# Kernel tuning notes

Measured on AMD Instinct MI355X. Metric: run time of the kernel, lower is better.

## Reference

```python
import jax, jax.numpy as jnp
import numpy as np

N = 100000   # nodes
E = 1000000  # edges
F = 16       # node features
FE = 4       # edge features
H = 8        # heads
C = 8        # hidden per head
HC = H * C   # 64
G = 64       # graphs in batch
NC = 4       # num classes
NS = 0.2     # negative slope
EPS = 1e-5


def setup_inputs() -> dict:
    key = jax.random.key(0)
    ks = list(jax.random.split(key, 40))
    it = iter(ks)
    nk = lambda shape, scale=0.1: jax.random.normal(next(it), shape, jnp.float32) * scale
    inp = {}
    inp["x"] = jax.random.normal(next(it), (N, F), jnp.float32)
    inp["edge_index"] = jax.random.randint(next(it), (2, E), 0, N, dtype=jnp.int64)
    inp["edge_attr"] = jax.random.normal(next(it), (E, FE), jnp.float32)
    inp["batch"] = jnp.sort(jax.random.randint(next(it), (N,), 0, G, dtype=jnp.int64))
    inp["g_n"] = jnp.ones((F,), jnp.float32); inp["b_n"] = jnp.zeros((F,), jnp.float32)
    inp["g_e"] = jnp.ones((FE,), jnp.float32); inp["b_e"] = jnp.zeros((FE,), jnp.float32)
    dims = [F, HC, HC]
    for i, d in enumerate(dims):
        inp[f"Wl{i}"] = nk((d, HC)); inp[f"bl{i}"] = jnp.zeros((HC,), jnp.float32)
        inp[f"Wr{i}"] = nk((d, HC)); inp[f"br{i}"] = jnp.zeros((HC,), jnp.float32)
        inp[f"We{i}"] = nk((FE, HC))
        inp[f"att{i}"] = nk((H, C))
        inp[f"bc{i}"] = jnp.zeros((HC,), jnp.float32)
    inp["t"] = jnp.ones((), jnp.float32)
    inp["W_out"] = nk((HC, NC)); inp["b_out"] = jnp.zeros((NC,), jnp.float32)
    return inp


def _bn(v, g, b):
    # torch BatchNorm1d training-mode forward: biased batch stats
    m = v.mean(0)
    var = jnp.var(v, 0)
    return (v - m) / jnp.sqrt(var + EPS) * g + b


def reference(x, edge_index, edge_attr, batch, g_n, b_n, g_e, b_e,
              Wl0, bl0, Wr0, br0, We0, att0, bc0,
              Wl1, bl1, Wr1, br1, We1, att1, bc1,
              Wl2, bl2, Wr2, br2, We2, att2, bc2,
              t, W_out, b_out):
    x = _bn(x, g_n, b_n)
    ea = _bn(edge_attr, g_e, b_e)
    src0, dst0 = edge_index[0], edge_index[1]
    # GATv2Conv default add_self_loops=True, fill_value='mean':
    # self-loop edge_attr = mean of incoming edge attrs per node (0 if none)
    cnt = jax.ops.segment_sum(jnp.ones((E,), jnp.float32), dst0, N)
    loop_attr = jax.ops.segment_sum(ea, dst0, N) / jnp.maximum(cnt, 1.0)[:, None]
    ar = jnp.arange(N, dtype=edge_index.dtype)
    src = jnp.concatenate([src0, ar])
    dst = jnp.concatenate([dst0, ar])
    ea_aug = jnp.concatenate([ea, loop_attr], 0)  # [E+N, FE]

    def conv(h, Wl, bl, Wr, br, We, att, bc):
        xl = (h @ Wl + bl).reshape(N, H, C)  # source transform
        xr = (h @ Wr + br).reshape(N, H, C)  # target transform
        ee = (ea_aug @ We).reshape(-1, H, C)
        m = jax.nn.leaky_relu(xl[src] + xr[dst] + ee, NS)  # [E+N, H, C]
        logits = jnp.einsum('ehc,hc->eh', m, att)
        amax = jax.ops.segment_max(logits, dst, N)  # every node has a self loop
        w = jnp.exp(logits - amax[dst])
        den = jax.ops.segment_sum(w, dst, N)
        alpha = w / den[dst]  # edge softmax per target node per head
        out = jax.ops.segment_sum(alpha[:, :, None] * xl[src], dst, N)
        return out.reshape(N, HC) + bc

    layers = [(Wl0, bl0, Wr0, br0, We0, att0, bc0),
              (Wl1, bl1, Wr1, br1, We1, att1, bc1),
              (Wl2, bl2, Wr2, br2, We2, att2, bc2)]
    for p in layers:
        x = jax.nn.leaky_relu(conv(x, *p), NS)

    # learnable softmax readout per graph, elementwise over channels
    s = x * t
    amax = jax.ops.segment_max(s, batch, G)
    w = jnp.exp(s - amax[batch])
    den = jax.ops.segment_sum(w, batch, G)
    agg = jax.ops.segment_sum((w / den[batch]) * x, batch, G)  # [G, HC]
    return agg @ W_out + b_out
```

## Files before the change

kernel.cpp:

```cpp
#include <hip/hip_runtime.h>
#include <math.h>

#define TPB 256
#define NBX 256
#define NBE 1024
#define CONVB 2048

typedef unsigned short u16;

__device__ __forceinline__ float lrelu(float v){ return fmaxf(v, 0.2f*v); }
#define RF(x) __builtin_amdgcn_readfirstlane(x)

__device__ __forceinline__ unsigned pack_bf16(float a, float b){
  unsigned ua = __float_as_uint(a), ub = __float_as_uint(b);
  ua = (ua + 0x7FFFu + ((ua >> 16) & 1u)) >> 16;
  ub = (ub + 0x7FFFu + ((ub >> 16) & 1u)) >> 16;
  return ua | (ub << 16);
}

__global__ __launch_bounds__(TPB) void k_stats_x(const float* __restrict__ x, float* __restrict__ px, int n){
  __shared__ float lds[4*32];
  int tid = blockIdx.x*blockDim.x + threadIdx.x;
  int stride = gridDim.x*blockDim.x;
  float s[16], q[16];
  #pragma unroll
  for (int i=0;i<16;++i){ s[i]=0.f; q[i]=0.f; }
  for (int r=tid; r<n; r+=stride){
    const float4* p = (const float4*)(x + (long)r*16);
    #pragma unroll
    for (int j=0;j<4;++j){
      float4 v = p[j];
      s[j*4+0]+=v.x; q[j*4+0]+=v.x*v.x;
      s[j*4+1]+=v.y; q[j*4+1]+=v.y*v.y;
      s[j*4+2]+=v.z; q[j*4+2]+=v.z*v.z;
      s[j*4+3]+=v.w; q[j*4+3]+=v.w*v.w;
    }
  }
  int wid = threadIdx.x >> 6, lane = threadIdx.x & 63;
  #pragma unroll
  for (int i=0;i<32;++i){
    float v = (i<16) ? s[i] : q[i-16];
    #pragma unroll
    for (int m=1;m<64;m<<=1) v += __shfl_xor(v, m);
    if (lane==0) lds[wid*32+i] = v;
  }
  __syncthreads();
  if (threadIdx.x < 32){
    float v = lds[threadIdx.x] + lds[32+threadIdx.x] + lds[64+threadIdx.x] + lds[96+threadIdx.x];
    px[blockIdx.x*32 + threadIdx.x] = v;
  }
}

__global__ __launch_bounds__(TPB) void k_edge0(const float* __restrict__ ea, const int* __restrict__ ei,
                      float* __restrict__ pe, int* __restrict__ cnt, int* __restrict__ rank, int E){
  __shared__ float lds[4*8];
  int tid = blockIdx.x*blockDim.x + threadIdx.x;
  int stride = gridDim.x*blockDim.x;
  float s[4]={0,0,0,0}, q[4]={0,0,0,0};
  for (int r=tid; r<E; r+=stride){
    float4 v = ((const float4*)ea)[r];
    s[0]+=v.x; q[0]+=v.x*v.x;
    s[1]+=v.y; q[1]+=v.y*v.y;
    s[2]+=v.z; q[2]+=v.z*v.z;
    s[3]+=v.w; q[3]+=v.w*v.w;
    int d = ei[E + r];
    rank[r] = atomicAdd(&cnt[d], 1);
  }
  int wid = threadIdx.x >> 6, lane = threadIdx.x & 63;
  #pragma unroll
  for (int i=0;i<8;++i){
    float v = (i<4) ? s[i] : q[i-4];
    #pragma unroll
    for (int m=1;m<64;m<<=1) v += __shfl_xor(v, m);
    if (lane==0) lds[wid*8+i] = v;
  }
  __syncthreads();
  if (threadIdx.x < 8){
    float v = lds[threadIdx.x] + lds[8+threadIdx.x] + lds[16+threadIdx.x] + lds[24+threadIdx.x];
    pe[blockIdx.x*8 + threadIdx.x] = v;
  }
}

__global__ __launch_bounds__(TPB) void k_finalize(const float* __restrict__ g_n, const float* __restrict__ b_n,
                           const float* __restrict__ g_e, const float* __restrict__ b_e,
                           const float* __restrict__ px, const float* __restrict__ pe,
                           float* __restrict__ st, int n, int e){
  __shared__ float lx[256], le[256];
  int t = threadIdx.x;
  {
    int c = t & 31, ch = t >> 5;
    float sx = 0.f;
    for (int b = ch*32; b < ch*32+32; ++b) sx += px[b*32 + c];
    lx[t] = sx;
  }
  {
    int c = t & 7, ch = t >> 3;
    float se = 0.f;
    for (int b = ch*32; b < ch*32+32; ++b) se += pe[b*8 + c];
    le[t] = se;
  }
  __syncthreads();
  if (t < 16){
    float sum = 0.f, sq = 0.f;
    #pragma unroll
    for (int ch=0; ch<8; ++ch){ sum += lx[ch*32 + t]; sq += lx[ch*32 + 16 + t]; }
    float mean = sum / (float)n;
    float var  = sq / (float)n - mean*mean;
    float sc = g_n[t] * rsqrtf(var + 1e-5f);
    st[40+t] = sc; st[56+t] = b_n[t] - mean*sc;
  } else if (t < 20){
    int f = t-16;
    float sum = 0.f, sq = 0.f;
    #pragma unroll
    for (int ch=0; ch<32; ++ch){ sum += le[ch*8 + f]; sq += le[ch*8 + 4 + f]; }
    float mean = sum / (float)e;
    float var  = sq / (float)e - mean*mean;
    float sc = g_e[f] * rsqrtf(var + 1e-5f);
    st[72+f] = sc; st[76+f] = b_e[f] - mean*sc;
  }
}

__global__ __launch_bounds__(TPB) void k_scan_a(const int* __restrict__ cnt, int* __restrict__ rp,
                                                int* __restrict__ part, int n){
  __shared__ int lds[TPB];
  int t = threadIdx.x;
  int base = blockIdx.x*2048 + t*8;
  int v[8]; int run = 0;
  #pragma unroll
  for (int j=0;j<8;++j){
    int idx = base + j;
    v[j] = run;
    run += (idx < n) ? cnt[idx] : 0;
  }
  lds[t] = run;
  __syncthreads();
  for (int off=1; off<TPB; off<<=1){
    int add = (t >= off) ? lds[t-off] : 0;
    __syncthreads();
    lds[t] += add;
    __syncthreads();
  }
  int excl = lds[t] - run;
  if (t == TPB-1) part[blockIdx.x] = lds[t];
  #pragma unroll
  for (int j=0;j<8;++j){
    int idx = base + j;
    if (idx < n) rp[idx] = v[j] + excl + idx;
  }
}

__global__ void k_scan_b(int* __restrict__ part, int nb){
  if (threadIdx.x==0 && blockIdx.x==0){
    int run = 0;
    for (int i=0;i<nb;++i){ int v = part[i]; part[i] = run; run += v; }
    part[nb] = run;
  }
}

__global__ __launch_bounds__(TPB) void k_scan_c(int* __restrict__ rp, const int* __restrict__ part, int n, int nb){
  int idx = blockIdx.x*blockDim.x + threadIdx.x;
  if (idx < n) rp[idx] += part[idx >> 11];
  else if (idx == n) rp[n] = part[nb] + n;
}

__global__ __launch_bounds__(TPB) void k_scatter(const int* __restrict__ ei, const int* __restrict__ rank,
                        const int* __restrict__ rp, int2* __restrict__ csr_se, int E){
  for (int e = blockIdx.x*blockDim.x + threadIdx.x; e < E; e += gridDim.x*blockDim.x){
    int srcv = ei[e];
    int d    = ei[E + e];
    int pos = rp[d] + rank[e];
    csr_se[pos] = make_int2(srcv, e);
  }
}

__global__ __launch_bounds__(TPB) void k_post(const int2* __restrict__ csr_se, const float4* __restrict__ ea,
                        const float* __restrict__ st, const int* __restrict__ rp,
                        int* __restrict__ csr_src, float4* __restrict__ csr_ea, int n){
  int lane = threadIdx.x & 63;
  int l16 = lane & 15;
  int node = (blockIdx.x*4 + (threadIdx.x >> 6))*4 + (lane >> 4);
  if (node >= n) return;
  float s0=st[72], s1=st[73], s2=st[74], s3=st[75];
  float h0=st[76], h1=st[77], h2=st[78], h3=st[79];
  int ib = rp[node], ie1 = rp[node+1] - 1;
  float4 sum = make_float4(0.f,0.f,0.f,0.f);
  for (int i = ib + l16; i < ie1; i += 16){
    int2 se = csr_se[i];
    float4 v = ea[se.y];
    float4 nv = make_float4(fmaf(v.x,s0,h0), fmaf(v.y,s1,h1), fmaf(v.z,s2,h2), fmaf(v.w,s3,h3));
    csr_src[i] = se.x;
    csr_ea[i] = nv;
    sum.x += nv.x; sum.y += nv.y; sum.z += nv.z; sum.w += nv.w;
  }
  #pragma unroll
  for (int m=1;m<16;m<<=1){
    sum.x += __shfl_xor(sum.x, m);
    sum.y += __shfl_xor(sum.y, m);
    sum.z += __shfl_xor(sum.z, m);
    sum.w += __shfl_xor(sum.w, m);
  }
  if (l16 == 0){
    int deg = ie1 - ib;
    float ic = 1.f / fmaxf((float)deg, 1.f);
    csr_src[ie1] = node;
    csr_ea[ie1] = make_float4(sum.x*ic, sum.y*ic, sum.z*ic, sum.w*ic);
  }
}

#define FMA16(i, xv) {                          \
    acc[i][0]  = fmaf(xv, wa.x, acc[i][0]);     \
    acc[i][1]  = fmaf(xv, wa.y, acc[i][1]);     \
    acc[i][2]  = fmaf(xv, wa.z, acc[i][2]);     \
    acc[i][3]  = fmaf(xv, wa.w, acc[i][3]);     \
    acc[i][4]  = fmaf(xv, wb.x, acc[i][4]);     \
    acc[i][5]  = fmaf(xv, wb.y, acc[i][5]);     \
    acc[i][6]  = fmaf(xv, wb.z, acc[i][6]);     \
    acc[i][7]  = fmaf(xv, wb.w, acc[i][7]);     \
    acc[i][8]  = fmaf(xv, wc.x, acc[i][8]);     \
    acc[i][9]  = fmaf(xv, wc.y, acc[i][9]);     \
    acc[i][10] = fmaf(xv, wc.z, acc[i][10]);    \
    acc[i][11] = fmaf(xv, wc.w, acc[i][11]);    \
    acc[i][12] = fmaf(xv, wd.x, acc[i][12]);    \
    acc[i][13] = fmaf(xv, wd.y, acc[i][13]);    \
    acc[i][14] = fmaf(xv, wd.z, acc[i][14]);    \
    acc[i][15] = fmaf(xv, wd.w, acc[i][15]); }
#define KSTEP(kk, c0_, c1_, c2_, c3_) {                                        \
    const float4* w4 = (const float4*)&Wlds[(k4*4+kk)*128 + c16];              \
    float4 wa = w4[0], wb = w4[1], wc = w4[2], wd = w4[3];                     \
    FMA16(0, c0_); FMA16(1, c1_); FMA16(2, c2_); FMA16(3, c3_); }

template<int K, bool BN>
__global__ __launch_bounds__(TPB) void k_gemm(const float* __restrict__ X,
    const float* __restrict__ Wl, const float* __restrict__ bl,
    const float* __restrict__ Wr, const float* __restrict__ br,
    const float* __restrict__ st,
    u16* __restrict__ xl, float* __restrict__ xr, int nrows){
  __shared__ __align__(16) float Wlds[K*128];
  __shared__ float blds[128];
  __shared__ float bns[16], bnb[16];
  int t = threadIdx.x;
  for (int idx = t; idx < K*128; idx += TPB){
    int k = idx >> 7, j = idx & 127;
    Wlds[idx] = (j < 64) ? Wl[k*64 + j] : Wr[k*64 + (j - 64)];
  }
  if (t < 64) blds[t] = bl[t];
  else if (t < 128) blds[t] = br[t - 64];
  if (BN){ if (t >= 128 && t < 144){ bns[t-128] = st[40 + (t-128)]; bnb[t-128] = st[56 + (t-128)]; } }
  __syncthreads();
  int rg = t & 31, c = t >> 5;
  int c16 = c*16;
  int r0 = blockIdx.x*128 + rg*4;
  int r[4];
  #pragma unroll
  for (int i=0;i<4;++i){ int ri = r0 + i; r[i] = (ri < nrows) ? ri : (nrows-1); }
  float acc[4][16];
  #pragma unroll
  for (int i=0;i<4;++i){
    #pragma unroll
    for (int j=0;j<16;++j) acc[i][j]=0.f;
  }
  #pragma unroll 2
  for (int k4=0; k4<K/4; ++k4){
    float4 xa = *(const float4*)&X[(size_t)r[0]*K + k4*4];
    float4 xb = *(const float4*)&X[(size_t)r[1]*K + k4*4];
    float4 xc = *(const float4*)&X[(size_t)r[2]*K + k4*4];
    float4 xd = *(const float4*)&X[(size_t)r[3]*K + k4*4];
    if (BN){
      float s0=bns[k4*4+0], b0=bnb[k4*4+0];
      float s1=bns[k4*4+1], b1=bnb[k4*4+1];
      float s2=bns[k4*4+2], b2=bnb[k4*4+2];
      float s3=bns[k4*4+3], b3=bnb[k4*4+3];
      xa.x=fmaf(xa.x,s0,b0); xa.y=fmaf(xa.y,s1,b1); xa.z=fmaf(xa.z,s2,b2); xa.w=fmaf(xa.w,s3,b3);
      xb.x=fmaf(xb.x,s0,b0); xb.y=fmaf(xb.y,s1,b1); xb.z=fmaf(xb.z,s2,b2); xb.w=fmaf(xb.w,s3,b3);
      xc.x=fmaf(xc.x,s0,b0); xc.y=fmaf(xc.y,s1,b1); xc.z=fmaf(xc.z,s2,b2); xc.w=fmaf(xc.w,s3,b3);
      xd.x=fmaf(xd.x,s0,b0); xd.y=fmaf(xd.y,s1,b1); xd.z=fmaf(xd.z,s2,b2); xd.w=fmaf(xd.w,s3,b3);
    }
    KSTEP(0, xa.x, xb.x, xc.x, xd.x);
    KSTEP(1, xa.y, xb.y, xc.y, xd.y);
    KSTEP(2, xa.z, xb.z, xc.z, xd.z);
    KSTEP(3, xa.w, xb.w, xc.w, xd.w);
  }
  if (c16 < 64){
    #pragma unroll
    for (int i=0;i<4;++i){
      if (r0 + i < nrows){
        u16* qb = &xl[(size_t)(r0+i)*64 + c16];
        uint4 p0, p1;
        p0.x = pack_bf16(acc[i][0] +blds[c16+0],  acc[i][1] +blds[c16+1]);
        p0.y = pack_bf16(acc[i][2] +blds[c16+2],  acc[i][3] +blds[c16+3]);
        p0.z = pack_bf16(acc[i][4] +blds[c16+4],  acc[i][5] +blds[c16+5]);
        p0.w = pack_bf16(acc[i][6] +blds[c16+6],  acc[i][7] +blds[c16+7]);
        p1.x = pack_bf16(acc[i][8] +blds[c16+8],  acc[i][9] +blds[c16+9]);
        p1.y = pack_bf16(acc[i][10]+blds[c16+10], acc[i][11]+blds[c16+11]);
        p1.z = pack_bf16(acc[i][12]+blds[c16+12], acc[i][13]+blds[c16+13]);
        p1.w = pack_bf16(acc[i][14]+blds[c16+14], acc[i][15]+blds[c16+15]);
        ((uint4*)qb)[0] = p0;
        ((uint4*)qb)[1] = p1;
      }
    }
  } else {
    int cb = c16 - 64;
    #pragma unroll
    for (int i=0;i<4;++i){
      if (r0 + i < nrows){
        float* q = &xr[(size_t)(r0+i)*64 + cb];
        ((float4*)q)[0] = make_float4(acc[i][0]+blds[c16+0],  acc[i][1]+blds[c16+1],
                                      acc[i][2]+blds[c16+2],  acc[i][3]+blds[c16+3]);
        ((float4*)q)[1] = make_float4(acc[i][4]+blds[c16+4],  acc[i][5]+blds[c16+5],
                                      acc[i][6]+blds[c16+6],  acc[i][7]+blds[c16+7]);
        ((float4*)q)[2] = make_float4(acc[i][8]+blds[c16+8],  acc[i][9]+blds[c16+9],
                                      acc[i][10]+blds[c16+10],acc[i][11]+blds[c16+11]);
        ((float4*)q)[3] = make_float4(acc[i][12]+blds[c16+12],acc[i][13]+blds[c16+13],
                                      acc[i][14]+blds[c16+14],acc[i][15]+blds[c16+15]);
      }
    }
  }
}

#define PROC(e_, a_, S_, O_) {                                              \
    float v = a_ + xrv;                                                     \
    v = fmaf(e_.x,we0, fmaf(e_.y,we1, fmaf(e_.z,we2, fmaf(e_.w,we3, v))));  \
    v = lrelu(v);                                                           \
    float p = v*attv;                                                       \
    p += __shfl_xor(p,1); p += __shfl_xor(p,2); p += __shfl_xor(p,4);       \
    float w_ = __expf(p);                                                   \
    S_ += w_; O_ = fmaf(w_, a_, O_); }
#define LOADSLOT(e_, a_, idx) { int s_ = RF(csr_src[idx]); e_ = csr_ea[idx]; \
    a_ = __uint_as_float(((unsigned)xl[(size_t)s_*64 + lane]) << 16); }

__global__ __launch_bounds__(TPB) void k_conv(
    const u16* __restrict__ xl, const float* __restrict__ xr,
    const int* __restrict__ rp, const int* __restrict__ csr_src, const float4* __restrict__ csr_ea,
    const float* __restrict__ We, const float* __restrict__ att, const float* __restrict__ bc,
    float* __restrict__ xout, int n){
  int lane = threadIdx.x & 63;
  int gw = blockIdx.x*4 + (threadIdx.x >> 6);
  int nw = gridDim.x*4;
  float we0 = We[lane], we1 = We[64+lane], we2 = We[128+lane], we3 = We[192+lane];
  float attv = att[lane];
  float bcv  = bc[lane];

  for (int node = gw; node < n; node += nw){
    int ib = RF(rp[node]);
    int ie = RF(rp[node+1]);
    float xrv = xr[(size_t)node*64 + lane];
    int ln = ie - ib;
    float S0=0.f, O0=0.f, S1=0.f, O1=0.f;
    float4 e0, e1, e2, e3, e4, e5;
    float a0=0.f, a1=0.f, a2=0.f, a3=0.f, a4=0.f, a5=0.f;
    LOADSLOT(e0, a0, ib);
    if (ln > 1) LOADSLOT(e1, a1, ib+1);
    if (ln > 2) LOADSLOT(e2, a2, ib+2);
    if (ln > 3) LOADSLOT(e3, a3, ib+3);
    if (ln > 4) LOADSLOT(e4, a4, ib+4);
    if (ln > 5) LOADSLOT(e5, a5, ib+5);
    int i = ib;
    for (; i+6 <= ie; i += 6){
      PROC(e0, a0, S0, O0); if (i+6  < ie) LOADSLOT(e0, a0, i+6);
      PROC(e1, a1, S1, O1); if (i+7  < ie) LOADSLOT(e1, a1, i+7);
      PROC(e2, a2, S0, O0); if (i+8  < ie) LOADSLOT(e2, a2, i+8);
      PROC(e3, a3, S1, O1); if (i+9  < ie) LOADSLOT(e3, a3, i+9);
      PROC(e4, a4, S0, O0); if (i+10 < ie) LOADSLOT(e4, a4, i+10);
      PROC(e5, a5, S1, O1); if (i+11 < ie) LOADSLOT(e5, a5, i+11);
    }
    int r = ie - i;
    if (r > 0) PROC(e0, a0, S0, O0);
    if (r > 1) PROC(e1, a1, S1, O1);
    if (r > 2) PROC(e2, a2, S0, O0);
    if (r > 3) PROC(e3, a3, S1, O1);
    if (r > 4) PROC(e4, a4, S0, O0);
    float o = (O0 + O1) / (S0 + S1) + bcv;
    xout[(size_t)node*64 + lane] = lrelu(o);
  }
}

__global__ __launch_bounds__(1024) void k_readout(const float* __restrict__ x,
    const int* __restrict__ batch, const float* __restrict__ tin,
    const float* __restrict__ Wout, const float* __restrict__ bout,
    float* __restrict__ out, int n){
  int g = blockIdx.x;
  int lane = threadIdx.x & 63, wid = threadIdx.x >> 6;
  int lo, hi;
  { int a=0, b=n; while (a<b){ int m=(a+b)>>1; if (batch[m] <  g) a=m+1; else b=m; } lo=a; }
  { int a=lo, b=n; while (a<b){ int m=(a+b)>>1; if (batch[m] <= g) a=m+1; else b=m; } hi=a; }
  float t = tin[0];
  __shared__ float red[16][64];
  float mx = -INFINITY;
  for (int nd = lo + wid; nd < hi; nd += 16)
    mx = fmaxf(mx, x[(size_t)nd*64 + lane]*t);
  red[wid][lane] = mx;
  __syncthreads();
  mx = -INFINITY;
  #pragma unroll
  for (int wv=0; wv<16; ++wv) mx = fmaxf(mx, red[wv][lane]);
  __syncthreads();
  float ld = 0.f, ln = 0.f;
  for (int nd = lo + wid; nd < hi; nd += 16){
    float xv = x[(size_t)nd*64 + lane];
    float w = __expf(xv*t - mx);
    ld += w; ln = fmaf(w, xv, ln);
  }
  red[wid][lane] = ld;
  __syncthreads();
  float den = 0.f;
  #pragma unroll
  for (int wv=0; wv<16; ++wv) den += red[wv][lane];
  __syncthreads();
  red[wid][lane] = ln;
  __syncthreads();
  if (wid == 0){
    float num = 0.f;
    #pragma unroll
    for (int wv=0; wv<16; ++wv) num += red[wv][lane];
    float agg = (hi > lo) ? num/den : 0.f;
    #pragma unroll
    for (int c=0;c<4;++c){
      float p = agg * Wout[lane*4 + c];
      #pragma unroll
      for (int m=1;m<64;m<<=1) p += __shfl_xor(p, m);
      if (lane == 0) out[g*4 + c] = p + bout[c];
    }
  }
}

extern "C" void kernel_launch(void* const* d_in, const int* in_sizes, int n_in,
                              void* d_out, int out_size, void* d_ws, size_t ws_size,
                              hipStream_t stream){
  const float* x     = (const float*)d_in[0];
  const int*   ei    = (const int*)d_in[1];
  const float* ea    = (const float*)d_in[2];
  const int*   batch = (const int*)d_in[3];
  const float* g_n = (const float*)d_in[4];
  const float* b_n = (const float*)d_in[5];
  const float* g_e = (const float*)d_in[6];
  const float* b_e = (const float*)d_in[7];
  const float* Wl[3]  = {(const float*)d_in[8],  (const float*)d_in[15], (const float*)d_in[22]};
  const float* bl[3]  = {(const float*)d_in[9],  (const float*)d_in[16], (const float*)d_in[23]};
  const float* Wr[3]  = {(const float*)d_in[10], (const float*)d_in[17], (const float*)d_in[24]};
  const float* br[3]  = {(const float*)d_in[11], (const float*)d_in[18], (const float*)d_in[25]};
  const float* We[3]  = {(const float*)d_in[12], (const float*)d_in[19], (const float*)d_in[26]};
  const float* att[3] = {(const float*)d_in[13], (const float*)d_in[20], (const float*)d_in[27]};
  const float* bc[3]  = {(const float*)d_in[14], (const float*)d_in[21], (const float*)d_in[28]};
  const float* tin  = (const float*)d_in[29];
  const float* Wout = (const float*)d_in[30];
  const float* bout = (const float*)d_in[31];
  float* out = (float*)d_out;

  const int n = in_sizes[0] / 16;
  const int E = in_sizes[1] / 2;

  char* w = (char*)d_ws;
  size_t off = 0;
  auto alloc = [&](size_t bytes)->char*{
    char* p = w + off;
    off = (off + bytes + 255) & ~(size_t)255;
    return p;
  };
  int*      cnt      = (int*)alloc((size_t)n*4);
  size_t zero_end = off;
  float*    st       = (float*)alloc(128*4);
  int*      rank     = (int*)alloc((size_t)E*4);
  float*    px       = (float*)alloc((size_t)NBX*32*4);
  float*    pe       = (float*)alloc((size_t)NBE*8*4);
  int*      rp       = (int*)alloc(((size_t)n+1)*4);
  int*      part     = (int*)alloc(64*4);
  int2*     csr_se   = (int2*)alloc((size_t)(E+n)*8);
  int*      csr_src  = (int*)alloc((size_t)(E+n)*4);
  float4*   csr_ea   = (float4*)alloc((size_t)(E+n)*16);
  u16*      xlb      = (u16*)alloc((size_t)n*64*2);
  float*    xrb      = (float*)alloc((size_t)n*64*4);
  float*    xbuf     = (float*)alloc((size_t)n*64*4);
  if (off > ws_size) return;

  hipMemsetAsync(d_ws, 0, zero_end, stream);

  k_stats_x<<<NBX, TPB, 0, stream>>>(x, px, n);
  k_edge0<<<NBE, TPB, 0, stream>>>(ea, ei, pe, cnt, rank, E);
  k_finalize<<<1, TPB, 0, stream>>>(g_n, b_n, g_e, b_e, px, pe, st, n, E);
  int nb = (n + 2047) / 2048;
  k_scan_a<<<nb, TPB, 0, stream>>>(cnt, rp, part, n);
  k_scan_b<<<1, 1, 0, stream>>>(part, nb);
  k_scan_c<<<(n + 1 + TPB - 1)/TPB, TPB, 0, stream>>>(rp, part, n, nb);
  k_scatter<<<2048, TPB, 0, stream>>>(ei, rank, rp, csr_se, E);
  k_post<<<(n + 15)/16, TPB, 0, stream>>>(csr_se, (const float4*)ea, st, rp, csr_src, (float4*)csr_ea, n);

  int gb = (n + 127)/128;
  for (int l=0; l<3; ++l){
    if (l == 0)
      k_gemm<16,true><<<gb, TPB, 0, stream>>>(x, Wl[0], bl[0], Wr[0], br[0], st, xlb, xrb, n);
    else
      k_gemm<64,false><<<gb, TPB, 0, stream>>>(xbuf, Wl[l], bl[l], Wr[l], br[l], st, xlb, xrb, n);
    k_conv<<<CONVB, TPB, 0, stream>>>(xlb, xrb, rp, csr_src, csr_ea,
                                      We[l], att[l], bc[l], xbuf, n);
  }

  k_readout<<<64, 1024, 0, stream>>>(xbuf, batch, tin, Wout, bout, out, n);
}
```

Before: 532.0 us.

## Process two edges per wavefront in conv by splitting lanes into half-waves

The attention-aggregation kernel now assigns each half of a 64-lane wavefront a different edge, with each lane handling two channels (packed bf16 pair loads, float2 xr). Partial sums from the two halves are combined with a cross-half shuffle at the end, and odd edge counts are handled by a masked tail. This doubles edges in flight per wave and halves the loop trip count, aiming to cut the latency-bound gather loop. In exchange each lane does more arithmetic per edge, source indices are no longer wave-uniform, and the final reduction adds shuffles.

```diff
diff --git a/kernel.cpp b/kernel.cpp
--- a/kernel.cpp
+++ b/kernel.cpp
@@ -317,16 +317,20 @@
   }
 }
 
-#define PROC(e_, a_, S_, O_) {                                              \
-    float v = a_ + xrv;                                                     \
-    v = fmaf(e_.x,we0, fmaf(e_.y,we1, fmaf(e_.z,we2, fmaf(e_.w,we3, v))));  \
-    v = lrelu(v);                                                           \
-    float p = v*attv;                                                       \
-    p += __shfl_xor(p,1); p += __shfl_xor(p,2); p += __shfl_xor(p,4);       \
-    float w_ = __expf(p);                                                   \
-    S_ += w_; O_ = fmaf(w_, a_, O_); }
-#define LOADSLOT(e_, a_, idx) { int s_ = RF(csr_src[idx]); e_ = csr_ea[idx]; \
-    a_ = __uint_as_float(((unsigned)xl[(size_t)s_*64 + lane]) << 16); }
+#define LOADP(e_, u_, i_) { int idx_ = (i_) + half; int s_ = csr_src[idx_];     \
+    e_ = csr_ea[idx_];                                                          \
+    u_ = *(const unsigned*)&xl[(size_t)s_*64 + (l32<<1)]; }
+#define PROCP(e_, u_) {                                                         \
+    float ax_ = __uint_as_float((u_) << 16);                                    \
+    float ay_ = __uint_as_float((u_) & 0xffff0000u);                            \
+    float v0_ = ax_ + xrx, v1_ = ay_ + xry;                                     \
+    v0_ = fmaf(e_.x,we0x, fmaf(e_.y,we1x, fmaf(e_.z,we2x, fmaf(e_.w,we3x, v0_))));\
+    v1_ = fmaf(e_.x,we0y, fmaf(e_.y,we1y, fmaf(e_.z,we2y, fmaf(e_.w,we3y, v1_))));\
+    v0_ = lrelu(v0_); v1_ = lrelu(v1_);                                         \
+    float p_ = fmaf(v0_, attx, v1_*atty);                                       \
+    p_ += __shfl_xor(p_,1); p_ += __shfl_xor(p_,2);                             \
+    float w_ = __expf(p_);                                                      \
+    S += w_; Ox = fmaf(w_,ax_,Ox); Oy = fmaf(w_,ay_,Oy); }
 
 __global__ __launch_bounds__(TPB) void k_conv(
     const u16* __restrict__ xl, const float* __restrict__ xr,
@@ -334,43 +338,65 @@
     const float* __restrict__ We, const float* __restrict__ att, const float* __restrict__ bc,
     float* __restrict__ xout, int n){
   int lane = threadIdx.x & 63;
+  int half = lane >> 5;
+  int l32  = lane & 31;
+  int c0 = l32*2, c1 = c0+1;
   int gw = blockIdx.x*4 + (threadIdx.x >> 6);
   int nw = gridDim.x*4;
-  float we0 = We[lane], we1 = We[64+lane], we2 = We[128+lane], we3 = We[192+lane];
-  float attv = att[lane];
-  float bcv  = bc[lane];
+  float we0x = We[c0],      we0y = We[c1];
+  float we1x = We[64+c0],   we1y = We[64+c1];
+  float we2x = We[128+c0],  we2y = We[128+c1];
+  float we3x = We[192+c0],  we3y = We[192+c1];
+  float attx = att[c0], atty = att[c1];
+  float bcx  = bc[c0],  bcy  = bc[c1];
 
   for (int node = gw; node < n; node += nw){
     int ib = RF(rp[node]);
     int ie = RF(rp[node+1]);
-    float xrv = xr[(size_t)node*64 + lane];
-    int ln = ie - ib;
-    float S0=0.f, O0=0.f, S1=0.f, O1=0.f;
-    float4 e0, e1, e2, e3, e4, e5;
-    float a0=0.f, a1=0.f, a2=0.f, a3=0.f, a4=0.f, a5=0.f;
-    LOADSLOT(e0, a0, ib);
-    if (ln > 1) LOADSLOT(e1, a1, ib+1);
-    if (ln > 2) LOADSLOT(e2, a2, ib+2);
-    if (ln > 3) LOADSLOT(e3, a3, ib+3);
-    if (ln > 4) LOADSLOT(e4, a4, ib+4);
-    if (ln > 5) LOADSLOT(e5, a5, ib+5);
+    int cnt = ie - ib;
+    float2 xrv = *(const float2*)&xr[(size_t)node*64 + c0];
+    float xrx = xrv.x, xry = xrv.y;
+    float S = 0.f, Ox = 0.f, Oy = 0.f;
+    float4 e0, e1, e2; unsigned u0=0, u1=0, u2=0;
+    int npf = cnt >> 1;
+    int iendf = ib + npf*2;
+    if (npf > 0) LOADP(e0,u0, ib);
+    if (npf > 1) LOADP(e1,u1, ib+2);
+    if (npf > 2) LOADP(e2,u2, ib+4);
     int i = ib;
-    for (; i+6 <= ie; i += 6){
-      PROC(e0, a0, S0, O0); if (i+6  < ie) LOADSLOT(e0, a0, i+6);
-      PROC(e1, a1, S1, O1); if (i+7  < ie) LOADSLOT(e1, a1, i+7);
-      PROC(e2, a2, S0, O0); if (i+8  < ie) LOADSLOT(e2, a2, i+8);
-      PROC(e3, a3, S1, O1); if (i+9  < ie) LOADSLOT(e3, a3, i+9);
-      PROC(e4, a4, S0, O0); if (i+10 < ie) LOADSLOT(e4, a4, i+10);
-      PROC(e5, a5, S1, O1); if (i+11 < ie) LOADSLOT(e5, a5, i+11);
-    }
-    int r = ie - i;
-    if (r > 0) PROC(e0, a0, S0, O0);
-    if (r > 1) PROC(e1, a1, S1, O1);
-    if (r > 2) PROC(e2, a2, S0, O0);
-    if (r > 3) PROC(e3, a3, S1, O1);
-    if (r > 4) PROC(e4, a4, S0, O0);
-    float o = (O0 + O1) / (S0 + S1) + bcv;
-    xout[(size_t)node*64 + lane] = lrelu(o);
+    for (; i+6 <= iendf; i += 6){
+      PROCP(e0,u0); if (i+6  < iendf) LOADP(e0,u0, i+6);
+      PROCP(e1,u1); if (i+8  < iendf) LOADP(e1,u1, i+8);
+      PROCP(e2,u2); if (i+10 < iendf) LOADP(e2,u2, i+10);
+    }
+    int rem = (iendf - i) >> 1;
+    if (rem > 0) PROCP(e0,u0);
+    if (rem > 1) PROCP(e1,u1);
+    if (cnt & 1){
+      int idx_ = min(iendf + half, ie - 1);
+      int s_ = csr_src[idx_];
+      float4 et = csr_ea[idx_];
+      unsigned ut = *(const unsigned*)&xl[(size_t)s_*64 + (l32<<1)];
+      float ax_ = __uint_as_float(ut << 16);
+      float ay_ = __uint_as_float(ut & 0xffff0000u);
+      float v0_ = ax_ + xrx, v1_ = ay_ + xry;
+      v0_ = fmaf(et.x,we0x, fmaf(et.y,we1x, fmaf(et.z,we2x, fmaf(et.w,we3x, v0_))));
+      v1_ = fmaf(et.x,we0y, fmaf(et.y,we1y, fmaf(et.z,we2y, fmaf(et.w,we3y, v1_))));
+      v0_ = lrelu(v0_); v1_ = lrelu(v1_);
+      float p_ = fmaf(v0_, attx, v1_*atty);
+      p_ += __shfl_xor(p_,1); p_ += __shfl_xor(p_,2);
+      float w_ = (half == 0) ? __expf(p_) : 0.f;
+      S += w_; Ox = fmaf(w_,ax_,Ox); Oy = fmaf(w_,ay_,Oy);
+    }
+    S  += __shfl_xor(S, 32);
+    Ox += __shfl_xor(Ox, 32);
+    Oy += __shfl_xor(Oy, 32);
+    if (half == 0){
+      float2 o;
+      o.x = lrelu(Ox / S + bcx);
+      o.y = lrelu(Oy / S + bcy);
+      *(float2*)&xout[(size_t)node*64 + c0] = o;
+    }
   }
 }
 
```

Measured after the change: 452.5 us. 14.9% less time.

## Process four edges per wavefront in GAT conv and fold scan stage into scan_c

Applied to the files above, without the earlier changes.

The conv kernel now splits each 64-lane wavefront into four 16-lane quarters. Each quarter handles a different edge and each lane covers 4 channels, loaded as a packed bf16 uint2, with the partial sums reduced across quarters by shuffles at the end. This cuts the per-edge shuffle chain and the serial dependency on one edge per wave, aiming for better memory-level parallelism on the gathers, in exchange for extra cross-quarter reductions and a masked remainder path. The single-thread k_scan_b launch is also removed: each thread in k_scan_c sums the block partials itself, which is cheap because there are only about 49 chunks.

```diff
diff --git a/kernel.cpp b/kernel.cpp
--- a/kernel.cpp
+++ b/kernel.cpp
@@ -149,18 +149,18 @@
   }
 }
 
-__global__ void k_scan_b(int* __restrict__ part, int nb){
-  if (threadIdx.x==0 && blockIdx.x==0){
-    int run = 0;
-    for (int i=0;i<nb;++i){ int v = part[i]; part[i] = run; run += v; }
-    part[nb] = run;
-  }
-}
-
 __global__ __launch_bounds__(TPB) void k_scan_c(int* __restrict__ rp, const int* __restrict__ part, int n, int nb){
   int idx = blockIdx.x*blockDim.x + threadIdx.x;
-  if (idx < n) rp[idx] += part[idx >> 11];
-  else if (idx == n) rp[n] = part[nb] + n;
+  if (idx < n){
+    int chunk = idx >> 11;
+    int add = 0;
+    for (int b = 0; b < chunk; ++b) add += part[b];
+    rp[idx] += add;
+  } else if (idx == n){
+    int tot = 0;
+    for (int b = 0; b < nb; ++b) tot += part[b];
+    rp[n] = tot + n;
+  }
 }
 
 __global__ __launch_bounds__(TPB) void k_scatter(const int* __restrict__ ei, const int* __restrict__ rank,
@@ -317,16 +317,27 @@
   }
 }
 
-#define PROC(e_, a_, S_, O_) {                                              \
-    float v = a_ + xrv;                                                     \
-    v = fmaf(e_.x,we0, fmaf(e_.y,we1, fmaf(e_.z,we2, fmaf(e_.w,we3, v))));  \
-    v = lrelu(v);                                                           \
-    float p = v*attv;                                                       \
-    p += __shfl_xor(p,1); p += __shfl_xor(p,2); p += __shfl_xor(p,4);       \
-    float w_ = __expf(p);                                                   \
-    S_ += w_; O_ = fmaf(w_, a_, O_); }
-#define LOADSLOT(e_, a_, idx) { int s_ = RF(csr_src[idx]); e_ = csr_ea[idx]; \
-    a_ = __uint_as_float(((unsigned)xl[(size_t)s_*64 + lane]) << 16); }
+#define LOADQ(e_, u_, i_) { int idx_ = (i_) + qq; int s_ = csr_src[idx_];       \
+    e_ = csr_ea[idx_];                                                          \
+    u_ = *(const uint2*)&xl[(size_t)s_*64 + (l16<<2)]; }
+#define PROCQ(e_, u_) {                                                         \
+    float a0_ = __uint_as_float((u_).x << 16);                                  \
+    float a1_ = __uint_as_float((u_).x & 0xffff0000u);                          \
+    float a2_ = __uint_as_float((u_).y << 16);                                  \
+    float a3_ = __uint_as_float((u_).y & 0xffff0000u);                          \
+    float v0_ = a0_ + xr4.x, v1_ = a1_ + xr4.y;                                 \
+    float v2_ = a2_ + xr4.z, v3_ = a3_ + xr4.w;                                 \
+    v0_ = fmaf(e_.x,we0.x, fmaf(e_.y,we1.x, fmaf(e_.z,we2.x, fmaf(e_.w,we3.x, v0_)))); \
+    v1_ = fmaf(e_.x,we0.y, fmaf(e_.y,we1.y, fmaf(e_.z,we2.y, fmaf(e_.w,we3.y, v1_)))); \
+    v2_ = fmaf(e_.x,we0.z, fmaf(e_.y,we1.z, fmaf(e_.z,we2.z, fmaf(e_.w,we3.z, v2_)))); \
+    v3_ = fmaf(e_.x,we0.w, fmaf(e_.y,we1.w, fmaf(e_.z,we2.w, fmaf(e_.w,we3.w, v3_)))); \
+    v0_=lrelu(v0_); v1_=lrelu(v1_); v2_=lrelu(v2_); v3_=lrelu(v3_);             \
+    float p_ = fmaf(v0_,att4.x, fmaf(v1_,att4.y, fmaf(v2_,att4.z, v3_*att4.w))); \
+    p_ += __shfl_xor(p_, 1);                                                    \
+    float w_ = __expf(p_);                                                      \
+    S += w_;                                                                    \
+    O0 = fmaf(w_,a0_,O0); O1 = fmaf(w_,a1_,O1);                                 \
+    O2 = fmaf(w_,a2_,O2); O3 = fmaf(w_,a3_,O3); }
 
 __global__ __launch_bounds__(TPB) void k_conv(
     const u16* __restrict__ xl, const float* __restrict__ xr,
@@ -334,43 +345,73 @@
     const float* __restrict__ We, const float* __restrict__ att, const float* __restrict__ bc,
     float* __restrict__ xout, int n){
   int lane = threadIdx.x & 63;
+  int qq  = lane >> 4;
+  int l16 = lane & 15;
+  int c0 = l16*4;
   int gw = blockIdx.x*4 + (threadIdx.x >> 6);
   int nw = gridDim.x*4;
-  float we0 = We[lane], we1 = We[64+lane], we2 = We[128+lane], we3 = We[192+lane];
-  float attv = att[lane];
-  float bcv  = bc[lane];
+  float4 we0 = *(const float4*)&We[c0];
+  float4 we1 = *(const float4*)&We[64+c0];
+  float4 we2 = *(const float4*)&We[128+c0];
+  float4 we3 = *(const float4*)&We[192+c0];
+  float4 att4 = *(const float4*)&att[c0];
+  float4 bc4  = *(const float4*)&bc[c0];
 
   for (int node = gw; node < n; node += nw){
     int ib = RF(rp[node]);
     int ie = RF(rp[node+1]);
-    float xrv = xr[(size_t)node*64 + lane];
-    int ln = ie - ib;
-    float S0=0.f, O0=0.f, S1=0.f, O1=0.f;
-    float4 e0, e1, e2, e3, e4, e5;
-    float a0=0.f, a1=0.f, a2=0.f, a3=0.f, a4=0.f, a5=0.f;
-    LOADSLOT(e0, a0, ib);
-    if (ln > 1) LOADSLOT(e1, a1, ib+1);
-    if (ln > 2) LOADSLOT(e2, a2, ib+2);
-    if (ln > 3) LOADSLOT(e3, a3, ib+3);
-    if (ln > 4) LOADSLOT(e4, a4, ib+4);
-    if (ln > 5) LOADSLOT(e5, a5, ib+5);
+    int cnt = ie - ib;
+    float4 xr4 = *(const float4*)&xr[(size_t)node*64 + c0];
+    float S = 0.f, O0 = 0.f, O1 = 0.f, O2 = 0.f, O3 = 0.f;
+    float4 e0, e1; uint2 u0 = {0,0}, u1 = {0,0};
+    int nq = cnt >> 2;
+    int iendf = ib + (nq << 2);
+    int rem = cnt & 3;
+    if (nq > 0) LOADQ(e0,u0, ib);
+    if (nq > 1) LOADQ(e1,u1, ib+4);
     int i = ib;
-    for (; i+6 <= ie; i += 6){
-      PROC(e0, a0, S0, O0); if (i+6  < ie) LOADSLOT(e0, a0, i+6);
-      PROC(e1, a1, S1, O1); if (i+7  < ie) LOADSLOT(e1, a1, i+7);
-      PROC(e2, a2, S0, O0); if (i+8  < ie) LOADSLOT(e2, a2, i+8);
-      PROC(e3, a3, S1, O1); if (i+9  < ie) LOADSLOT(e3, a3, i+9);
-      PROC(e4, a4, S0, O0); if (i+10 < ie) LOADSLOT(e4, a4, i+10);
-      PROC(e5, a5, S1, O1); if (i+11 < ie) LOADSLOT(e5, a5, i+11);
-    }
-    int r = ie - i;
-    if (r > 0) PROC(e0, a0, S0, O0);
-    if (r > 1) PROC(e1, a1, S1, O1);
-    if (r > 2) PROC(e2, a2, S0, O0);
-    if (r > 3) PROC(e3, a3, S1, O1);
-    if (r > 4) PROC(e4, a4, S0, O0);
-    float o = (O0 + O1) / (S0 + S1) + bcv;
-    xout[(size_t)node*64 + lane] = lrelu(o);
+    for (; i+8 <= iendf; i += 8){
+      PROCQ(e0,u0); if (i+8  < iendf) LOADQ(e0,u0, i+8);
+      PROCQ(e1,u1); if (i+12 < iendf) LOADQ(e1,u1, i+12);
+    }
+    if (iendf - i >= 4) PROCQ(e0,u0);
+    if (rem){
+      int idx_ = min(iendf + qq, ie - 1);
+      int s_ = csr_src[idx_];
+      float4 et = csr_ea[idx_];
+      uint2 ut = *(const uint2*)&xl[(size_t)s_*64 + (l16<<2)];
+      float a0_ = __uint_as_float(ut.x << 16);
+      float a1_ = __uint_as_float(ut.x & 0xffff0000u);
+      float a2_ = __uint_as_float(ut.y << 16);
+      float a3_ = __uint_as_float(ut.y & 0xffff0000u);
+      float v0_ = a0_ + xr4.x, v1_ = a1_ + xr4.y;
+      float v2_ = a2_ + xr4.z, v3_ = a3_ + xr4.w;
+      v0_ = fmaf(et.x,we0.x, fmaf(et.y,we1.x, fmaf(et.z,we2.x, fmaf(et.w,we3.x, v0_))));
+      v1_ = fmaf(et.x,we0.y, fmaf(et.y,we1.y, fmaf(et.z,we2.y, fmaf(et.w,we3.y, v1_))));
+      v2_ = fmaf(et.x,we0.z, fmaf(et.y,we1.z, fmaf(et.z,we2.z, fmaf(et.w,we3.z, v2_))));
+      v3_ = fmaf(et.x,we0.w, fmaf(et.y,we1.w, fmaf(et.z,we2.w, fmaf(et.w,we3.w, v3_))));
+      v0_=lrelu(v0_); v1_=lrelu(v1_); v2_=lrelu(v2_); v3_=lrelu(v3_);
+      float p_ = fmaf(v0_,att4.x, fmaf(v1_,att4.y, fmaf(v2_,att4.z, v3_*att4.w)));
+      p_ += __shfl_xor(p_, 1);
+      float w_ = (qq < rem) ? __expf(p_) : 0.f;
+      S += w_;
+      O0 = fmaf(w_,a0_,O0); O1 = fmaf(w_,a1_,O1);
+      O2 = fmaf(w_,a2_,O2); O3 = fmaf(w_,a3_,O3);
+    }
+    S  += __shfl_xor(S, 16);  S  += __shfl_xor(S, 32);
+    O0 += __shfl_xor(O0,16);  O0 += __shfl_xor(O0,32);
+    O1 += __shfl_xor(O1,16);  O1 += __shfl_xor(O1,32);
+    O2 += __shfl_xor(O2,16);  O2 += __shfl_xor(O2,32);
+    O3 += __shfl_xor(O3,16);  O3 += __shfl_xor(O3,32);
+    if (qq == 0){
+      float inv = 1.f / S;
+      float4 o;
+      o.x = lrelu(fmaf(O0, inv, bc4.x));
+      o.y = lrelu(fmaf(O1, inv, bc4.y));
+      o.z = lrelu(fmaf(O2, inv, bc4.z));
+      o.w = lrelu(fmaf(O3, inv, bc4.w));
+      *(float4*)&xout[(size_t)node*64 + c0] = o;
+    }
   }
 }
 
@@ -479,7 +520,6 @@
   k_finalize<<<1, TPB, 0, stream>>>(g_n, b_n, g_e, b_e, px, pe, st, n, E);
   int nb = (n + 2047) / 2048;
   k_scan_a<<<nb, TPB, 0, stream>>>(cnt, rp, part, n);
-  k_scan_b<<<1, 1, 0, stream>>>(part, nb);
   k_scan_c<<<(n + 1 + TPB - 1)/TPB, TPB, 0, stream>>>(rp, part, n, nb);
   k_scatter<<<2048, TPB, 0, stream>>>(ei, rank, rp, csr_se, E);
   k_post<<<(n + 15)/16, TPB, 0, stream>>>(csr_se, (const float4*)ea, st, rp, csr_src, (float4*)csr_ea, n);
```

Result: faster. 486.1 us (-8.6%).
